# Performance work log

Measured on AMD Instinct MI355X. Metric: run time of the kernel, lower is better.

The kernel has to match this reference:

```python
import jax, jax.numpy as jnp
import numpy as np

B, S, D = 4, 2048, 1024
NEG = 1e9


def setup_inputs() -> dict:
    key = jax.random.key(0)
    ks = jax.random.split(key, 4)
    scale = 1.0 / np.sqrt(D)  # glorot-ish init scale for stability
    x = jax.random.normal(ks[0], (B, S, D), dtype=jnp.float32)
    Wq = jax.random.normal(ks[1], (D, D), dtype=jnp.float32) * scale
    Wk = jax.random.normal(ks[2], (D, D), dtype=jnp.float32) * scale
    Wv = jax.random.normal(ks[3], (D, D), dtype=jnp.float32) * scale
    bq = jnp.zeros((D,), jnp.float32)
    bk = jnp.zeros((D,), jnp.float32)
    bv = jnp.zeros((D,), jnp.float32)
    return {"x": x, "Wq": Wq, "bq": bq, "Wk": Wk, "bk": bk, "Wv": Wv, "bv": bv}


def reference(x, Wq, bq, Wk, bk, Wv, bv):
    # Dense projections (single head, no 1/sqrt(d) scaling, matching source)
    q = x @ Wq + bq                      # [B,S,D]
    k = x @ Wk + bk                      # [B,S,D]
    v = x @ Wv + bv                      # [B,S,D]
    scores = jnp.einsum('bqd,bkd->bqk', q, k)   # [B,S,S]
    seq = scores.shape[-1]
    mask = jnp.tril(jnp.ones((seq, seq), scores.dtype))  # lower-triangular causal
    scores = scores * mask - NEG * (1.0 - mask)
    weights = jax.nn.softmax(scores, axis=-1)
    return jnp.einsum('bqk,bkd->bqd', weights, v)
```

## Files before the change

### kernel.cpp

```cpp
#include <hip/hip_runtime.h>

typedef float f32x4  __attribute__((ext_vector_type(4)));
typedef _Float16 f16x8  __attribute__((ext_vector_type(8)));
typedef _Float16 f16x4v __attribute__((ext_vector_type(4)));
typedef _Float16 f16x8v __attribute__((ext_vector_type(8)));

__device__ inline void load_lds16(const _Float16* g, _Float16* l) {
    __builtin_amdgcn_global_load_lds((const __attribute__((address_space(1))) void*)g,
                                     (__attribute__((address_space(3))) void*)l, 16, 0, 0);
}

__global__ __launch_bounds__(256)
void convert_h(const float* __restrict__ X, _Float16* __restrict__ H, long n4)
{
    long i = (long)blockIdx.x * 256 + threadIdx.x;
    if (i >= n4) return;
    f32x4 v = ((const f32x4*)X)[i];
    f16x4v h;
#pragma unroll
    for (int k = 0; k < 4; ++k) h[k] = (_Float16)v[k];
    ((f16x4v*)H)[i] = h;
}

__global__ __launch_bounds__(256)
void transpose_w3(const float* __restrict__ Wq, const float* __restrict__ Wk,
                  const float* __restrict__ Wv,
                  _Float16* __restrict__ Hqk, _Float16* __restrict__ Lqk,
                  _Float16* __restrict__ Hv, int D)
{
    const int z = blockIdx.z;
    const float* W = (z == 0) ? Wq : (z == 1) ? Wk : Wv;
    _Float16* Th = (z == 0) ? Hqk : (z == 1) ? Hqk + (long)D * D : Hv;
    _Float16* Tl = (z == 0) ? Lqk : (z == 1) ? Lqk + (long)D * D : nullptr;

    __shared__ float t[32][33];
    const int tid = threadIdx.x;
    const int bx = blockIdx.x * 32, by = blockIdx.y * 32;
    const int c = tid & 31, r0 = tid >> 5;
#pragma unroll
    for (int r = r0; r < 32; r += 8)
        t[r][c] = W[(long)(by + r) * D + bx + c];
    __syncthreads();
#pragma unroll
    for (int r = r0; r < 32; r += 8) {
        float v = t[c][r];
        _Float16 h = (_Float16)v;
        Th[(long)(bx + r) * D + by + c] = h;
        if (z < 2) Tl[(long)(bx + r) * D + by + c] = (_Float16)(v - (float)h);
    }
}

constexpr int TM = 128, TK = 32;

__global__ __launch_bounds__(256)
void proj_fused(const _Float16* __restrict__ x_h,
                const _Float16* __restrict__ Wqk_h, const _Float16* __restrict__ Wqk_l,
                const _Float16* __restrict__ Wv_h,
                _Float16* __restrict__ Q_h, _Float16* __restrict__ K_h,
                _Float16* __restrict__ K_l, _Float16* __restrict__ Vt,
                const float* __restrict__ bq, const float* __restrict__ bk,
                const float* __restrict__ bv)
{
    constexpr int D = 1024, SEQ = 2048;
    const int ct = blockIdx.x, rt = blockIdx.y;
    const bool qk = ct < 16;
    const int row0 = rt * TM;
    const int col0 = (qk ? ct : ct - 16) * TM;

    __shared__ __align__(16) _Float16 smem[16384];
    _Float16* sA  = smem;
    _Float16* sBh = smem + 4096;
    _Float16* sBl = smem + 8192;

    const int tid = threadIdx.x;
    const int lane = tid & 63, wave = tid >> 6;
    const int l16 = lane & 15, quad = lane >> 4;
    const int wm = (wave >> 1) * 64, wn = (wave & 1) * 64;

    f32x4 acc[4][4] = {};

    if (qk) {
        for (int k0 = 0; k0 < D; k0 += TK) {
#pragma unroll
            for (int rnd = 0; rnd < 2; ++rnd) {
                const int row = rnd * 64 + (tid >> 2);
                const long gA = (long)(row0 + row) * D + k0 + (tid & 3) * 8;
                const long gB = (long)(col0 + row) * D + k0 + (tid & 3) * 8;
                const int lofs = rnd * 2048 + tid * 8;
                load_lds16(x_h + gA, sA + lofs);
                load_lds16(Wqk_h + gB, sBh + lofs);
                load_lds16(Wqk_l + gB, sBl + lofs);
            }
            __syncthreads();
            f16x8 a[4], b_h[4], b_l[4];
#pragma unroll
            for (int i = 0; i < 4; ++i)
                a[i] = *(const f16x8*)&sA[(wm + i * 16 + l16) * TK + (quad << 3)];
#pragma unroll
            for (int j = 0; j < 4; ++j) {
                b_h[j] = *(const f16x8*)&sBh[(wn + j * 16 + l16) * TK + (quad << 3)];
                b_l[j] = *(const f16x8*)&sBl[(wn + j * 16 + l16) * TK + (quad << 3)];
            }
#pragma unroll
            for (int i = 0; i < 4; ++i)
#pragma unroll
                for (int j = 0; j < 4; ++j) {
                    acc[i][j] = __builtin_amdgcn_mfma_f32_16x16x32_f16(a[i], b_h[j], acc[i][j], 0, 0, 0);
                    acc[i][j] = __builtin_amdgcn_mfma_f32_16x16x32_f16(a[i], b_l[j], acc[i][j], 0, 0, 0);
                }
            __syncthreads();
        }
        const bool isQ = col0 < D;
#pragma unroll
        for (int j = 0; j < 4; ++j) {
            const int col = col0 + wn + j * 16 + l16;
            const int cc = isQ ? col : col - D;
            const float bval = isQ ? bq[cc] : bk[cc];
#pragma unroll
            for (int i = 0; i < 4; ++i) {
                const int rb = row0 + wm + i * 16 + quad * 4;
#pragma unroll
                for (int r = 0; r < 4; ++r) {
                    const float v = acc[i][j][r] + bval;
                    const _Float16 h = (_Float16)v;
                    if (isQ) {
                        Q_h[(long)(rb + r) * D + cc] = h;
                    } else {
                        K_h[(long)(rb + r) * D + cc] = h;
                        K_l[(long)(rb + r) * D + cc] = (_Float16)(v - (float)h);
                    }
                }
            }
        }
    } else {
        for (int k0 = 0; k0 < D; k0 += TK) {
#pragma unroll
            for (int rnd = 0; rnd < 2; ++rnd) {
                const int row = rnd * 64 + (tid >> 2);
                const long gA = (long)(row0 + row) * D + k0 + (tid & 3) * 8;
                const long gB = (long)(col0 + row) * D + k0 + (tid & 3) * 8;
                const int lofs = rnd * 2048 + tid * 8;
                load_lds16(x_h + gA, sA + lofs);
                load_lds16(Wv_h + gB, sBh + lofs);
            }
            __syncthreads();
            f16x8 a[4], b[4];
#pragma unroll
            for (int i = 0; i < 4; ++i)
                a[i] = *(const f16x8*)&sA[(wm + i * 16 + l16) * TK + (quad << 3)];
#pragma unroll
            for (int j = 0; j < 4; ++j)
                b[j] = *(const f16x8*)&sBh[(wn + j * 16 + l16) * TK + (quad << 3)];
#pragma unroll
            for (int i = 0; i < 4; ++i)
#pragma unroll
                for (int j = 0; j < 4; ++j)
                    acc[i][j] = __builtin_amdgcn_mfma_f32_16x16x32_f16(a[i], b[j], acc[i][j], 0, 0, 0);
            __syncthreads();
        }
        _Float16* sVt = smem;
#pragma unroll
        for (int j = 0; j < 4; ++j) {
            const int cl_ = wn + j * 16 + l16;
            const float bval = bv[col0 + cl_];
#pragma unroll
            for (int i = 0; i < 4; ++i) {
#pragma unroll
                for (int r = 0; r < 4; ++r) {
                    const int sl = wm + i * 16 + quad * 4 + r;
                    sVt[cl_ * TM + (sl ^ ((cl_ & 15) << 3))] = (_Float16)(acc[i][j][r] + bval);
                }
            }
        }
        __syncthreads();
        const int bb = row0 / SEQ;
        const int sbase = row0 - bb * SEQ;
        for (int idx = tid; idx < TM * TM / 8; idx += 256) {
            const int cl_ = idx >> 4, s0 = (idx & 15) << 3;
            f16x8v v = *(const f16x8v*)&sVt[cl_ * TM + (s0 ^ ((cl_ & 15) << 3))];
            *(f16x8v*)&Vt[(long)bb * D * SEQ + (long)(col0 + cl_) * SEQ + sbase + s0] = v;
        }
    }
}

template<bool BLO, int MODE, int TNB>
__global__ __launch_bounds__(256)
void gemm2(const _Float16* __restrict__ Ah, long sA, int lda,
           const _Float16* __restrict__ Bh, const _Float16* __restrict__ Bl,
           long sB, int ldb,
           float* __restrict__ Cf, long sC, int ldc, int K)
{
    static_assert(MODE != 1 || TNB == 64, "packed causal decode assumes TNB=64");
    constexpr int NFJ = TNB / 32;
    constexpr int BRNDS = TNB / 64;

    int rt, ct;
    if (MODE == 1) {
        const int t = blockIdx.x;
        rt = (int)((sqrtf(4.0f * t + 1.0f) - 1.0f) * 0.5f);
        while (rt * (rt + 1) > t) --rt;
        while ((rt + 1) * (rt + 2) <= t) ++rt;
        ct = t - rt * (rt + 1);
    } else {
        rt = (gridDim.x - 1) - blockIdx.x;
        ct = blockIdx.y;
    }
    const int bz = blockIdx.z;

    const _Float16* gAh = Ah + (long)bz * sA;
    const _Float16* gBh = Bh + (long)bz * sB;
    const _Float16* gBl = BLO ? Bl + (long)bz * sB : nullptr;

    const int row0 = rt * TM, col0 = ct * TNB;
    const int k_end = (MODE == 2) ? min(K, (rt + 1) * TM) : K;

    __shared__ _Float16 sAh[TM * TK];
    __shared__ _Float16 sBh[TNB * TK];
    __shared__ _Float16 sBl[BLO ? TNB * TK : 8];

    const int tid = threadIdx.x;
    const int lane = tid & 63, wave = tid >> 6;
    const int l16 = lane & 15, quad = lane >> 4;
    const int wm = (wave >> 1) * 64, wn = (wave & 1) * (TNB / 2);

    f32x4 acc[4][NFJ] = {};

    for (int k0 = 0; k0 < k_end; k0 += TK) {
#pragma unroll
        for (int rnd = 0; rnd < 2; ++rnd) {
            const int row = rnd * 64 + (tid >> 2);
            const long gA = (long)(row0 + row) * lda + k0 + (tid & 3) * 8;
            load_lds16(gAh + gA, sAh + rnd * 2048 + tid * 8);
        }
#pragma unroll
        for (int rnd = 0; rnd < BRNDS; ++rnd) {
            const int row = rnd * 64 + (tid >> 2);
            const long gB = (long)(col0 + row) * ldb + k0 + (tid & 3) * 8;
            const int lofs = rnd * 2048 + tid * 8;
            load_lds16(gBh + gB, sBh + lofs);
            if (BLO) load_lds16(gBl + gB, sBl + lofs);
        }
        __syncthreads();

        f16x8 a[4], b_h[NFJ];
#pragma unroll
        for (int i = 0; i < 4; ++i)
            a[i] = *(const f16x8*)&sAh[(wm + i * 16 + l16) * TK + (quad << 3)];
#pragma unroll
        for (int j = 0; j < NFJ; ++j)
            b_h[j] = *(const f16x8*)&sBh[(wn + j * 16 + l16) * TK + (quad << 3)];

        if (BLO) {
            f16x8 b_l[NFJ];
#pragma unroll
            for (int j = 0; j < NFJ; ++j)
                b_l[j] = *(const f16x8*)&sBl[(wn + j * 16 + l16) * TK + (quad << 3)];
#pragma unroll
            for (int i = 0; i < 4; ++i)
#pragma unroll
                for (int j = 0; j < NFJ; ++j) {
                    acc[i][j] = __builtin_amdgcn_mfma_f32_16x16x32_f16(a[i], b_h[j], acc[i][j], 0, 0, 0);
                    acc[i][j] = __builtin_amdgcn_mfma_f32_16x16x32_f16(a[i], b_l[j], acc[i][j], 0, 0, 0);
                }
        } else {
#pragma unroll
            for (int i = 0; i < 4; ++i)
#pragma unroll
                for (int j = 0; j < NFJ; ++j)
                    acc[i][j] = __builtin_amdgcn_mfma_f32_16x16x32_f16(a[i], b_h[j], acc[i][j], 0, 0, 0);
        }
        __syncthreads();
    }

    float* cf = Cf + (long)bz * sC;
#pragma unroll
    for (int j = 0; j < NFJ; ++j) {
        const int col = col0 + wn + j * 16 + l16;
#pragma unroll
        for (int i = 0; i < 4; ++i) {
            const int rb = row0 + wm + i * 16 + quad * 4;
#pragma unroll
            for (int r = 0; r < 4; ++r)
                cf[(long)(rb + r) * ldc + col] = acc[i][j][r];
        }
    }
}

__global__ __launch_bounds__(256)
void softmax_kernel(const float* __restrict__ Sc, _Float16* __restrict__ P, int seq)
{
    const int r = blockIdx.x, b = blockIdx.y;
    const float* row = Sc + ((long)b * seq + r) * seq;
    _Float16* prow = P + ((long)b * seq + r) * seq;
    const int tid = threadIdx.x;
    const int cmax = ((r >> 7) + 1) << 7;
    const int c0 = tid * 8;

    float v[8];
    f32x4 v0, v1;
    if (c0 <= r) {
        const f32x4* rp = (const f32x4*)row;
        v0 = rp[tid * 2];
        v1 = rp[tid * 2 + 1];
    } else {
        v0 = (f32x4)(-3.0e38f);
        v1 = (f32x4)(-3.0e38f);
    }
    float lmax = -3.0e38f;
#pragma unroll
    for (int k = 0; k < 4; ++k) {
        v[k]     = (c0 + k     <= r) ? v0[k] : -3.0e38f;
        v[k + 4] = (c0 + k + 4 <= r) ? v1[k] : -3.0e38f;
    }
#pragma unroll
    for (int k = 0; k < 8; ++k) lmax = fmaxf(lmax, v[k]);

    __shared__ float red[256];
    red[tid] = lmax; __syncthreads();
    for (int s = 128; s > 0; s >>= 1) {
        if (tid < s) red[tid] = fmaxf(red[tid], red[tid + s]);
        __syncthreads();
    }
    const float m = red[0];
    __syncthreads();

    float lsum = 0.0f;
#pragma unroll
    for (int k = 0; k < 8; ++k) {
        float e = (v[k] > -1.0e38f) ? __expf(v[k] - m) : 0.0f;
        v[k] = e;
        lsum += e;
    }
    red[tid] = lsum; __syncthreads();
    for (int s = 128; s > 0; s >>= 1) {
        if (tid < s) red[tid] += red[tid + s];
        __syncthreads();
    }
    const float inv = 1.0f / red[0];

    if (c0 < cmax) {
        f16x8v o;
#pragma unroll
        for (int k = 0; k < 8; ++k) o[k] = (_Float16)(v[k] * inv);
        ((f16x8v*)prow)[tid] = o;
    }
}

extern "C" void kernel_launch(void* const* d_in, const int* in_sizes, int n_in,
                              void* d_out, int out_size, void* d_ws, size_t ws_size,
                              hipStream_t stream)
{
    constexpr int B = 4, S = 2048, D = 1024;
    constexpr long MB = 1024 * 1024;
    const float* x  = (const float*)d_in[0];
    const float* Wq = (const float*)d_in[1];
    const float* bq = (const float*)d_in[2];
    const float* Wk = (const float*)d_in[3];
    const float* bk = (const float*)d_in[4];
    const float* Wv = (const float*)d_in[5];
    const float* bv = (const float*)d_in[6];
    float* out = (float*)d_out;

    char* ws = (char*)d_ws;
    _Float16* x_h    = (_Float16*)(ws + 0);
    _Float16* Wqkt_h = (_Float16*)(ws + 16 * MB);
    _Float16* Wqkt_l = (_Float16*)(ws + 20 * MB);
    _Float16* Wvt_h  = (_Float16*)(ws + 24 * MB);
    float*    Sc     = (float*)(ws + 0);
    _Float16* Q_h    = (_Float16*)(ws + 64 * MB);
    _Float16* K_h    = (_Float16*)(ws + 80 * MB);
    _Float16* K_l    = (_Float16*)(ws + 96 * MB);
    _Float16* Vt     = (_Float16*)(ws + 112 * MB);
    _Float16* P      = (_Float16*)(ws + 128 * MB);

    const int M = B * S;
    dim3 blk(256);

    convert_h<<<(M * D / 4 + 255) / 256, blk, 0, stream>>>(x, x_h, (long)M * D / 4);
    transpose_w3<<<dim3(D / 32, D / 32, 3), blk, 0, stream>>>(
        Wq, Wk, Wv, Wqkt_h, Wqkt_l, Wvt_h, D);

    proj_fused<<<dim3(24, M / TM), blk, 0, stream>>>(
        x_h, Wqkt_h, Wqkt_l, Wvt_h, Q_h, K_h, K_l, Vt, bq, bk, bv);

    const int ntiles = (S / TM) * (S / TM + 1);
    gemm2<true, 1, 64><<<dim3(ntiles, 1, B), blk, 0, stream>>>(
        Q_h, (long)S * D, D, K_h, K_l, (long)S * D, D,
        Sc, (long)S * S, S, D);

    softmax_kernel<<<dim3(S, B), blk, 0, stream>>>(Sc, P, S);

    gemm2<false, 2, 64><<<dim3(S / TM, D / 64, B), blk, 0, stream>>>(
        P, (long)S * S, S, Vt, nullptr, (long)D * S, S,
        out, (long)S * D, D, S);
}
```

Measured before the change: 339.8 us.

## Rewrite QKV projection as 256x256-tile double-buffered GEMM with packed hi/lo weights

Replaces the 128x128, 256-thread projection kernel with a 512-thread kernel that computes 256x256 output tiles. The LDS staging is double-buffered and XOR-swizzled, and MFMA work is interleaved with async global-to-LDS prefetch under explicit waitcnt and barrier scheduling. The Q/K weight hi and lo halves are stored as one concatenated K dimension, so the split-precision product becomes a single longer K loop instead of two MFMAs per step. Block indices are remapped for cache locality. The goal is more reuse per tile and hidden load latency, at the cost of 128KB of LDS per block, which limits occupancy, and more complex synchronization.

```diff
diff --git a/kernel.cpp b/kernel.cpp
--- a/kernel.cpp
+++ b/kernel.cpp
@@ -25,13 +25,10 @@
 __global__ __launch_bounds__(256)
 void transpose_w3(const float* __restrict__ Wq, const float* __restrict__ Wk,
                   const float* __restrict__ Wv,
-                  _Float16* __restrict__ Hqk, _Float16* __restrict__ Lqk,
-                  _Float16* __restrict__ Hv, int D)
+                  _Float16* __restrict__ W2, _Float16* __restrict__ Wvt, int D)
 {
     const int z = blockIdx.z;
     const float* W = (z == 0) ? Wq : (z == 1) ? Wk : Wv;
-    _Float16* Th = (z == 0) ? Hqk : (z == 1) ? Hqk + (long)D * D : Hv;
-    _Float16* Tl = (z == 0) ? Lqk : (z == 1) ? Lqk + (long)D * D : nullptr;
 
     __shared__ float t[32][33];
     const int tid = threadIdx.x;
@@ -45,83 +42,143 @@
     for (int r = r0; r < 32; r += 8) {
         float v = t[c][r];
         _Float16 h = (_Float16)v;
-        Th[(long)(bx + r) * D + by + c] = h;
-        if (z < 2) Tl[(long)(bx + r) * D + by + c] = (_Float16)(v - (float)h);
-    }
-}
-
-constexpr int TM = 128, TK = 32;
-
-__global__ __launch_bounds__(256)
-void proj_fused(const _Float16* __restrict__ x_h,
-                const _Float16* __restrict__ Wqk_h, const _Float16* __restrict__ Wqk_l,
-                const _Float16* __restrict__ Wv_h,
-                _Float16* __restrict__ Q_h, _Float16* __restrict__ K_h,
-                _Float16* __restrict__ K_l, _Float16* __restrict__ Vt,
-                const float* __restrict__ bq, const float* __restrict__ bk,
-                const float* __restrict__ bv)
-{
-    constexpr int D = 1024, SEQ = 2048;
-    const int ct = blockIdx.x, rt = blockIdx.y;
-    const bool qk = ct < 16;
-    const int row0 = rt * TM;
-    const int col0 = (qk ? ct : ct - 16) * TM;
-
-    __shared__ __align__(16) _Float16 smem[16384];
-    _Float16* sA  = smem;
-    _Float16* sBh = smem + 4096;
-    _Float16* sBl = smem + 8192;
+        if (z < 2) {
+            const long nrow = (long)z * D + bx + r;
+            W2[nrow * 2 * D + by + c]     = h;
+            W2[nrow * 2 * D + D + by + c] = (_Float16)(v - (float)h);
+        } else {
+            Wvt[(long)(bx + r) * D + by + c] = h;
+        }
+    }
+}
+
+__global__ __launch_bounds__(512, 2)
+void proj8(const _Float16* __restrict__ x_h, const _Float16* __restrict__ W2,
+           const _Float16* __restrict__ Wvt,
+           _Float16* __restrict__ Q_h, _Float16* __restrict__ K_h,
+           _Float16* __restrict__ K_l, _Float16* __restrict__ Vt,
+           const float* __restrict__ bq, const float* __restrict__ bk,
+           const float* __restrict__ bv)
+{
+    constexpr int D = 1024, SEQ = 2048, BK = 64;
+    __shared__ __align__(16) _Float16 lds[65536];
+
+    const int orig = blockIdx.x;
+    const int bij = (orig & 7) * 48 + (orig >> 3);
+    const bool isV = bij >= 256;
+    int ct, rt, ldb, NT;
+    const _Float16* Bb;
+    if (!isV) { ct = bij & 7;  rt = bij >> 3;         Bb = W2;  ldb = 2 * D; NT = 32; }
+    else      { const int b2 = bij - 256;
+                ct = b2 & 3;   rt = b2 >> 2;          Bb = Wvt; ldb = D;     NT = 16; }
+    const int row0 = rt * 256, col0 = ct * 256;
 
     const int tid = threadIdx.x;
-    const int lane = tid & 63, wave = tid >> 6;
-    const int l16 = lane & 15, quad = lane >> 4;
-    const int wm = (wave >> 1) * 64, wn = (wave & 1) * 64;
-
-    f32x4 acc[4][4] = {};
-
-    if (qk) {
-        for (int k0 = 0; k0 < D; k0 += TK) {
-#pragma unroll
-            for (int rnd = 0; rnd < 2; ++rnd) {
-                const int row = rnd * 64 + (tid >> 2);
-                const long gA = (long)(row0 + row) * D + k0 + (tid & 3) * 8;
-                const long gB = (long)(col0 + row) * D + k0 + (tid & 3) * 8;
-                const int lofs = rnd * 2048 + tid * 8;
-                load_lds16(x_h + gA, sA + lofs);
-                load_lds16(Wqk_h + gB, sBh + lofs);
-                load_lds16(Wqk_l + gB, sBl + lofs);
-            }
-            __syncthreads();
-            f16x8 a[4], b_h[4], b_l[4];
-#pragma unroll
-            for (int i = 0; i < 4; ++i)
-                a[i] = *(const f16x8*)&sA[(wm + i * 16 + l16) * TK + (quad << 3)];
-#pragma unroll
-            for (int j = 0; j < 4; ++j) {
-                b_h[j] = *(const f16x8*)&sBh[(wn + j * 16 + l16) * TK + (quad << 3)];
-                b_l[j] = *(const f16x8*)&sBl[(wn + j * 16 + l16) * TK + (quad << 3)];
-            }
-#pragma unroll
-            for (int i = 0; i < 4; ++i)
-#pragma unroll
-                for (int j = 0; j < 4; ++j) {
-                    acc[i][j] = __builtin_amdgcn_mfma_f32_16x16x32_f16(a[i], b_h[j], acc[i][j], 0, 0, 0);
-                    acc[i][j] = __builtin_amdgcn_mfma_f32_16x16x32_f16(a[i], b_l[j], acc[i][j], 0, 0, 0);
+    const int wave = tid >> 6, lane = tid & 63, l16 = lane & 15, quad = lane >> 4;
+    const int wn = (wave & 3) * 32;
+
+    _Float16* SA = lds;
+    _Float16* SB = lds + 32768;
+
+#define STAGEH(gb, ld, grow0, gk, dst)                                          \
+    {                                                                           \
+        _Pragma("unroll")                                                       \
+        for (int q_ = 0; q_ < 2; ++q_) {                                        \
+            const int p_ = q_ * 512 + tid;                                      \
+            const int rw_ = p_ >> 3;                                            \
+            const int kq_ = (p_ & 7) ^ (rw_ & 7);                               \
+            load_lds16((gb) + (long)((grow0) + rw_) * (ld) + (gk) + kq_ * 8,    \
+                       (dst) + p_ * 8);                                         \
+        }                                                                       \
+    }
+
+    STAGEH(Bb, ldb, col0,       0, SB);
+    STAGEH(Bb, ldb, col0 + 128, 0, SB + 8192);
+    STAGEH(x_h, D, row0,        0, SA);
+    STAGEH(x_h, D, row0 + 128,  0, SA + 8192);
+    asm volatile("s_waitcnt vmcnt(0)" ::: "memory");
+    __syncthreads();
+
+    f32x4 acc[16][2] = {};
+
+    for (int t = 0; t < NT; ++t) {
+        const int cur = t & 1;
+        _Float16* Ac = SA + cur * 16384;
+        _Float16* Bc = SB + cur * 16384 + (wave >> 2) * 8192;
+        _Float16* An = SA + (cur ^ 1) * 16384;
+        _Float16* Bn = SB + (cur ^ 1) * 16384;
+        const bool pf = (t + 1 < NT);
+        const int kA = ((t + 1) * BK) & (D - 1);
+        const int kB = (t + 1) * BK;
+
+        f16x8 b[2][2];
+#pragma unroll
+        for (int p = 0; p < 4; ++p) {
+            f16x8 a[4][2];
+#pragma unroll
+            for (int il = 0; il < 4; ++il) {
+                const int lr = (p & 1) * 64 + il * 16 + l16;
+#pragma unroll
+                for (int kk = 0; kk < 2; ++kk)
+                    a[il][kk] = *(const f16x8*)&Ac[(p >> 1) * 8192 + lr * 64 +
+                                    ((((kk << 2) | quad) ^ (lr & 7)) << 3)];
+            }
+            if (p == 0) {
+#pragma unroll
+                for (int j = 0; j < 2; ++j) {
+                    const int nr = wn + j * 16 + l16;
+#pragma unroll
+                    for (int kk = 0; kk < 2; ++kk)
+                        b[j][kk] = *(const f16x8*)&Bc[nr * 64 +
+                                        ((((kk << 2) | quad) ^ (nr & 7)) << 3)];
                 }
-            __syncthreads();
-        }
-        const bool isQ = col0 < D;
-#pragma unroll
-        for (int j = 0; j < 4; ++j) {
-            const int col = col0 + wn + j * 16 + l16;
-            const int cc = isQ ? col : col - D;
-            const float bval = isQ ? bq[cc] : bk[cc];
-#pragma unroll
-            for (int i = 0; i < 4; ++i) {
-                const int rb = row0 + wm + i * 16 + quad * 4;
+            }
+            if (pf) {
+                if (p == 0) STAGEH(Bb, ldb, col0,       kB, Bn);
+                if (p == 1) STAGEH(Bb, ldb, col0 + 128, kB, Bn + 8192);
+                if (p == 2) STAGEH(x_h, D, row0,        kA, An);
+                if (p == 3) STAGEH(x_h, D, row0 + 128,  kA, An + 8192);
+            }
+            if (p == 1) {
+                if (pf) asm volatile("s_waitcnt vmcnt(4)" ::: "memory");
+                else    asm volatile("s_waitcnt vmcnt(0)" ::: "memory");
+            }
+            if (p == 3) {
+                if (pf) asm volatile("s_waitcnt vmcnt(2)" ::: "memory");
+                else    asm volatile("s_waitcnt vmcnt(0)" ::: "memory");
+            }
+            __builtin_amdgcn_s_barrier();
+            asm volatile("s_waitcnt lgkmcnt(0)" ::: "memory");
+            __builtin_amdgcn_sched_barrier(0);
+            __builtin_amdgcn_s_setprio(1);
+#pragma unroll
+            for (int il = 0; il < 4; ++il)
+#pragma unroll
+                for (int j = 0; j < 2; ++j)
+#pragma unroll
+                    for (int kk = 0; kk < 2; ++kk)
+                        acc[p * 4 + il][j] = __builtin_amdgcn_mfma_f32_16x16x32_f16(
+                            a[il][kk], b[j][kk], acc[p * 4 + il][j], 0, 0, 0);
+            __builtin_amdgcn_s_setprio(0);
+            __builtin_amdgcn_s_barrier();
+        }
+    }
+
+    if (!isV) {
+        const bool isQ = ct < 4;
+        const float* bias = isQ ? bq : bk;
+        const int cw = col0 + wave * 32;
+#pragma unroll
+        for (int j = 0; j < 2; ++j) {
+            const int colg = cw + j * 16 + l16;
+            const int cc = isQ ? colg : colg - D;
+            const float bval = bias[cc];
+#pragma unroll
+            for (int ig = 0; ig < 16; ++ig) {
+                const int rb = row0 + ig * 16 + quad * 4;
 #pragma unroll
                 for (int r = 0; r < 4; ++r) {
-                    const float v = acc[i][j][r] + bval;
+                    const float v = acc[ig][j][r] + bval;
                     const _Float16 h = (_Float16)v;
                     if (isQ) {
                         Q_h[(long)(rb + r) * D + cc] = h;
@@ -133,55 +190,35 @@
             }
         }
     } else {
-        for (int k0 = 0; k0 < D; k0 += TK) {
-#pragma unroll
-            for (int rnd = 0; rnd < 2; ++rnd) {
-                const int row = rnd * 64 + (tid >> 2);
-                const long gA = (long)(row0 + row) * D + k0 + (tid & 3) * 8;
-                const long gB = (long)(col0 + row) * D + k0 + (tid & 3) * 8;
-                const int lofs = rnd * 2048 + tid * 8;
-                load_lds16(x_h + gA, sA + lofs);
-                load_lds16(Wv_h + gB, sBh + lofs);
-            }
-            __syncthreads();
-            f16x8 a[4], b[4];
-#pragma unroll
-            for (int i = 0; i < 4; ++i)
-                a[i] = *(const f16x8*)&sA[(wm + i * 16 + l16) * TK + (quad << 3)];
-#pragma unroll
-            for (int j = 0; j < 4; ++j)
-                b[j] = *(const f16x8*)&sBh[(wn + j * 16 + l16) * TK + (quad << 3)];
-#pragma unroll
-            for (int i = 0; i < 4; ++i)
-#pragma unroll
-                for (int j = 0; j < 4; ++j)
-                    acc[i][j] = __builtin_amdgcn_mfma_f32_16x16x32_f16(a[i], b[j], acc[i][j], 0, 0, 0);
-            __syncthreads();
-        }
-        _Float16* sVt = smem;
-#pragma unroll
-        for (int j = 0; j < 4; ++j) {
-            const int cl_ = wn + j * 16 + l16;
-            const float bval = bv[col0 + cl_];
-#pragma unroll
-            for (int i = 0; i < 4; ++i) {
-#pragma unroll
-                for (int r = 0; r < 4; ++r) {
-                    const int sl = wm + i * 16 + quad * 4 + r;
-                    sVt[cl_ * TM + (sl ^ ((cl_ & 15) << 3))] = (_Float16)(acc[i][j][r] + bval);
-                }
+        _Float16* sVt = lds;
+        const int cw = wave * 32;
+#pragma unroll
+        for (int j = 0; j < 2; ++j) {
+            const int cl = cw + j * 16 + l16;
+            const float bval = bv[col0 + cl];
+#pragma unroll
+            for (int ig = 0; ig < 16; ++ig) {
+                f16x4v pk;
+#pragma unroll
+                for (int r = 0; r < 4; ++r) pk[r] = (_Float16)(acc[ig][j][r] + bval);
+                const int sb = cl * 512 + ((ig * 32 + quad * 8) ^ ((cl & 31) << 4));
+                *(f16x4v*)((char*)sVt + sb) = pk;
             }
         }
         __syncthreads();
-        const int bb = row0 / SEQ;
-        const int sbase = row0 - bb * SEQ;
-        for (int idx = tid; idx < TM * TM / 8; idx += 256) {
-            const int cl_ = idx >> 4, s0 = (idx & 15) << 3;
-            f16x8v v = *(const f16x8v*)&sVt[cl_ * TM + (s0 ^ ((cl_ & 15) << 3))];
-            *(f16x8v*)&Vt[(long)bb * D * SEQ + (long)(col0 + cl_) * SEQ + sbase + s0] = v;
-        }
-    }
-}
+        const int bb = row0 >> 11;
+        const int s0 = row0 & (SEQ - 1);
+        for (int idx = tid; idx < 8192; idx += 512) {
+            const int cl = idx >> 5, r8 = idx & 31;
+            const int sb = cl * 512 + ((r8 * 16) ^ ((cl & 31) << 4));
+            f16x8v v = *(const f16x8v*)((char*)sVt + sb);
+            *(f16x8v*)&Vt[((long)bb * D + col0 + cl) * SEQ + s0 + r8 * 8] = v;
+        }
+    }
+#undef STAGEH
+}
+
+constexpr int TM = 128, TK = 32;
 
 template<bool BLO, int MODE, int TNB>
 __global__ __launch_bounds__(256)
@@ -362,26 +399,25 @@
     float* out = (float*)d_out;
 
     char* ws = (char*)d_ws;
-    _Float16* x_h    = (_Float16*)(ws + 0);
-    _Float16* Wqkt_h = (_Float16*)(ws + 16 * MB);
-    _Float16* Wqkt_l = (_Float16*)(ws + 20 * MB);
-    _Float16* Wvt_h  = (_Float16*)(ws + 24 * MB);
-    float*    Sc     = (float*)(ws + 0);
-    _Float16* Q_h    = (_Float16*)(ws + 64 * MB);
-    _Float16* K_h    = (_Float16*)(ws + 80 * MB);
-    _Float16* K_l    = (_Float16*)(ws + 96 * MB);
-    _Float16* Vt     = (_Float16*)(ws + 112 * MB);
-    _Float16* P      = (_Float16*)(ws + 128 * MB);
+    _Float16* x_h   = (_Float16*)(ws + 0);
+    _Float16* W2    = (_Float16*)(ws + 16 * MB);
+    _Float16* Wvt_h = (_Float16*)(ws + 24 * MB);
+    float*    Sc    = (float*)(ws + 0);
+    _Float16* Q_h   = (_Float16*)(ws + 64 * MB);
+    _Float16* K_h   = (_Float16*)(ws + 80 * MB);
+    _Float16* K_l   = (_Float16*)(ws + 96 * MB);
+    _Float16* Vt    = (_Float16*)(ws + 112 * MB);
+    _Float16* P     = (_Float16*)(ws + 128 * MB);
 
     const int M = B * S;
     dim3 blk(256);
 
     convert_h<<<(M * D / 4 + 255) / 256, blk, 0, stream>>>(x, x_h, (long)M * D / 4);
     transpose_w3<<<dim3(D / 32, D / 32, 3), blk, 0, stream>>>(
-        Wq, Wk, Wv, Wqkt_h, Wqkt_l, Wvt_h, D);
-
-    proj_fused<<<dim3(24, M / TM), blk, 0, stream>>>(
-        x_h, Wqkt_h, Wqkt_l, Wvt_h, Q_h, K_h, K_l, Vt, bq, bk, bv);
+        Wq, Wk, Wv, W2, Wvt_h, D);
+
+    proj8<<<dim3(384), dim3(512), 0, stream>>>(
+        x_h, W2, Wvt_h, Q_h, K_h, K_l, Vt, bq, bk, bv);
 
     const int ntiles = (S / TM) * (S / TM + 1);
     gemm2<true, 1, 64><<<dim3(ntiles, 1, B), blk, 0, stream>>>(
```

Measured after the change: 407.0 us. +19.8%, slower.
